# Performance work log

Hardware: AMD Instinct MI355X
Metric: run time of the kernel (lower is better)

Reference implementation:

```python
import jax, jax.numpy as jnp
import numpy as np

# Model dims: N = polynomial degree, RANK = CP rank, HxW image, S = flattened size
N, RANK, H, W = 4, 128, 256, 256
S = H * W
B = 32
EPS = 1e-5  # torch BatchNorm2d default eps


def setup_inputs() -> dict:
    key = jax.random.key(0)
    ks = jax.random.split(key, 4)
    x = jax.random.normal(ks[0], (B, 1, H, W), dtype=jnp.float32)
    # PolyLayer (PolyGAN CCP) parameters: per-degree factors U_n [S, RANK],
    # output projection C [S, RANK], output bias beta [S]
    U = jax.random.normal(ks[1], (N, S, RANK), dtype=jnp.float32) * 0.02
    C = jax.random.normal(ks[2], (S, RANK), dtype=jnp.float32) * 0.02
    beta = jax.random.normal(ks[3], (S,), dtype=jnp.float32) * 0.02
    # BatchNorm2d(1) affine params (torch default init: weight=1, bias=0)
    gamma = jnp.ones((1,), dtype=jnp.float32)
    bn_bias = jnp.zeros((1,), dtype=jnp.float32)
    return {"x": x, "U": U, "C": C, "beta": beta, "gamma": gamma, "bn_bias": bn_bias}


def reference(x, U, C, beta, gamma, bn_bias):
    b = x.shape[0]
    # BatchNorm2d(num_features=1), training mode: biased batch stats over (N,H,W)
    mean = jnp.mean(x, axis=(0, 2, 3), keepdims=True)
    var = jnp.var(x, axis=(0, 2, 3), keepdims=True)
    xn = (x - mean) * jax.lax.rsqrt(var + EPS)
    xn = xn * gamma.reshape(1, -1, 1, 1) + bn_bias.reshape(1, -1, 1, 1)
    # Flatten each sample: [B, S]. The torch Generator applies PolyLayer
    # per-sample across Python threads; here it is one batched call.
    z = xn.reshape(b, S)
    # CCP polynomial: t_n = U_n^T z for each degree -> [N, B, RANK]
    t = jnp.einsum('bs,nsr->nbr', z, U)
    h = t[0]
    for n in range(1, N):  # fixed small degree loop (structural, not data dim)
        h = t[n] * h + h   # h_n = (U_n^T z) * h_{n-1} + h_{n-1}
    out = h @ C.T + beta   # project back to image space: [B, S]
    return out.reshape(b, 1, H, W)
```

## Files before the change

### kernel.cpp

```cpp
#include <hip/hip_runtime.h>

#define SDIM 65536
#define BDIM 32
#define RDIM 128
#define NDEG 4
#define NCHUNK 256
#define CHUNK_S (SDIM / NCHUNK)
#define MTOT (BDIM * SDIM)
#define EPS_BN 1e-5f
#define NSTATB 512

__global__ void k_stats(const float* __restrict__ x, float* __restrict__ partial) {
    __shared__ float s_sum[256];
    __shared__ float s_sq[256];
    int tid = threadIdx.x;
    int gid = blockIdx.x * 256 + tid;
    int stride = gridDim.x * 256;
    float sum = 0.f, sq = 0.f;
    const float4* x4 = (const float4*)x;
    for (int i = gid; i < MTOT / 4; i += stride) {
        float4 v = x4[i];
        sum += (v.x + v.y) + (v.z + v.w);
        sq  += (v.x * v.x + v.y * v.y) + (v.z * v.z + v.w * v.w);
    }
    s_sum[tid] = sum; s_sq[tid] = sq;
    __syncthreads();
    for (int off = 128; off > 0; off >>= 1) {
        if (tid < off) { s_sum[tid] += s_sum[tid + off]; s_sq[tid] += s_sq[tid + off]; }
        __syncthreads();
    }
    if (tid == 0) { partial[blockIdx.x * 2] = s_sum[0]; partial[blockIdx.x * 2 + 1] = s_sq[0]; }
}

__global__ void k_stats_fin(const float* __restrict__ partial, float* __restrict__ stats) {
    __shared__ float s_sum[256];
    __shared__ float s_sq[256];
    int tid = threadIdx.x;
    float sum = partial[tid * 2] + partial[(tid + 256) * 2];
    float sq  = partial[tid * 2 + 1] + partial[(tid + 256) * 2 + 1];
    s_sum[tid] = sum; s_sq[tid] = sq;
    __syncthreads();
    for (int off = 128; off > 0; off >>= 1) {
        if (tid < off) { s_sum[tid] += s_sum[tid + off]; s_sq[tid] += s_sq[tid + off]; }
        __syncthreads();
    }
    if (tid == 0) { stats[0] = s_sum[0]; stats[1] = s_sq[0]; }
}

__global__ void __launch_bounds__(256) k_norm_t(const float* __restrict__ x,
                                                const float* __restrict__ gamma,
                                                const float* __restrict__ bnb,
                                                const float* __restrict__ stats,
                                                float* __restrict__ zT) {
    __shared__ float lds[64][33];
    int tid = threadIdx.x;
    int s0 = blockIdx.x * 64;
    float mean = stats[0] * (1.f / MTOT);
    float var  = stats[1] * (1.f / MTOT) - mean * mean;
    float istd = rsqrtf(var + EPS_BN);
    float a  = gamma[0] * istd;
    float c0 = bnb[0] - mean * a;

    int sl = tid & 63, bq = tid >> 6;
#pragma unroll
    for (int k = 0; k < 8; ++k) {
        int b = k * 4 + bq;
        lds[sl][b] = fmaf(a, x[(size_t)b * SDIM + s0 + sl], c0);
    }
    __syncthreads();
    int bl = tid & 31, sq = tid >> 5;
#pragma unroll
    for (int k = 0; k < 8; ++k) {
        int s = k * 8 + sq;
        zT[(size_t)(s0 + s) * BDIM + bl] = lds[s][bl];
    }
}

__global__ void __launch_bounds__(256) k_gemm_t(const float* __restrict__ zT,
                                                const float* __restrict__ U,
                                                float* __restrict__ t_part) {
    __shared__ float lds_z[CHUNK_S * BDIM];
    int tid  = threadIdx.x;
    int p    = tid & 63;
    int o    = __builtin_amdgcn_readfirstlane(tid >> 6);
    int chunk = blockIdx.x;
    int n     = blockIdx.y;
    int s0 = chunk * CHUNK_S;

    {
        const float4* src4 = (const float4*)(zT + (size_t)s0 * BDIM);
        float4* dst4 = (float4*)lds_z;
#pragma unroll
        for (int i = 0; i < (CHUNK_S * BDIM / 4) / 256; ++i)
            dst4[i * 256 + tid] = src4[i * 256 + tid];
    }
    __syncthreads();

    const float* Ub = U + (size_t)n * SDIM * RDIM + (size_t)s0 * RDIM;
    const float4* zq = (const float4*)lds_z;

    float acc[8][2];
#pragma unroll
    for (int j = 0; j < 8; ++j) { acc[j][0] = 0.f; acc[j][1] = 0.f; }

#pragma unroll 2
    for (int s = 0; s < CHUNK_S; ++s) {
        float4 z0 = zq[s * (BDIM / 4) + o * 2];
        float4 z1 = zq[s * (BDIM / 4) + o * 2 + 1];
        float2 u2 = *(const float2*)(Ub + (size_t)s * RDIM + 2 * p);
        acc[0][0] = fmaf(z0.x, u2.x, acc[0][0]); acc[0][1] = fmaf(z0.x, u2.y, acc[0][1]);
        acc[1][0] = fmaf(z0.y, u2.x, acc[1][0]); acc[1][1] = fmaf(z0.y, u2.y, acc[1][1]);
        acc[2][0] = fmaf(z0.z, u2.x, acc[2][0]); acc[2][1] = fmaf(z0.z, u2.y, acc[2][1]);
        acc[3][0] = fmaf(z0.w, u2.x, acc[3][0]); acc[3][1] = fmaf(z0.w, u2.y, acc[3][1]);
        acc[4][0] = fmaf(z1.x, u2.x, acc[4][0]); acc[4][1] = fmaf(z1.x, u2.y, acc[4][1]);
        acc[5][0] = fmaf(z1.y, u2.x, acc[5][0]); acc[5][1] = fmaf(z1.y, u2.y, acc[5][1]);
        acc[6][0] = fmaf(z1.z, u2.x, acc[6][0]); acc[6][1] = fmaf(z1.z, u2.y, acc[6][1]);
        acc[7][0] = fmaf(z1.w, u2.x, acc[7][0]); acc[7][1] = fmaf(z1.w, u2.y, acc[7][1]);
    }

    float* outp = t_part + ((size_t)n * NCHUNK + chunk) * (BDIM * RDIM);
#pragma unroll
    for (int j = 0; j < 8; ++j) {
        int b = o * 8 + j;
        *(float2*)(outp + b * RDIM + 2 * p) = make_float2(acc[j][0], acc[j][1]);
    }
}

__global__ void __launch_bounds__(256) k_reduce_h(const float* __restrict__ t_part,
                                                  float* __restrict__ h) {
    __shared__ float lds[NDEG][8][32];
    int tid = threadIdx.x;
    int il = tid & 31;
    int cg = tid >> 5;
    int i0 = blockIdx.x * 32;

#pragma unroll
    for (int n = 0; n < NDEG; ++n) {
        float s = 0.f;
#pragma unroll 4
        for (int k = 0; k < 32; ++k) {
            int c = cg * 32 + k;
            s += t_part[(size_t)(n * NCHUNK + c) * (BDIM * RDIM) + i0 + il];
        }
        lds[n][cg][il] = s;
    }
    __syncthreads();
    if (tid < 32) {
        float t[NDEG];
#pragma unroll
        for (int n = 0; n < NDEG; ++n) {
            float s = 0.f;
#pragma unroll
            for (int g = 0; g < 8; ++g) s += lds[n][g][il];
            t[n] = s;
        }
        float hh = t[0];
#pragma unroll
        for (int n = 1; n < NDEG; ++n) hh = fmaf(t[n], hh, hh);
        h[i0 + il] = hh;
    }
}

__global__ void __launch_bounds__(256) k_out(const float* __restrict__ h,
                                             const float* __restrict__ Cm,
                                             const float* __restrict__ beta,
                                             float* __restrict__ out) {
    int tid = threadIdx.x;
    int s   = (blockIdx.x >> 1) * 64 + (tid & 63);
    int bg  = __builtin_amdgcn_readfirstlane((blockIdx.x & 1) * 4 + (tid >> 6));
    int b0  = bg * 4;

    float acc[4] = {0.f, 0.f, 0.f, 0.f};
    const float4* Cr = (const float4*)(Cm + (size_t)s * RDIM);
    const float* hb = h + b0 * RDIM;

#pragma unroll 8
    for (int rc = 0; rc < RDIM / 4; ++rc) {
        float4 c = Cr[rc];
#pragma unroll
        for (int j = 0; j < 4; ++j) {
            const float* hr = hb + j * RDIM + rc * 4;
            float a = acc[j];
            a = fmaf(c.x, hr[0], a);
            a = fmaf(c.y, hr[1], a);
            a = fmaf(c.z, hr[2], a);
            a = fmaf(c.w, hr[3], a);
            acc[j] = a;
        }
    }
    float bt = beta[s];
#pragma unroll
    for (int j = 0; j < 4; ++j)
        out[(size_t)(b0 + j) * SDIM + s] = acc[j] + bt;
}

extern "C" void kernel_launch(void* const* d_in, const int* in_sizes, int n_in,
                              void* d_out, int out_size, void* d_ws, size_t ws_size,
                              hipStream_t stream) {
    const float* x     = (const float*)d_in[0];
    const float* U     = (const float*)d_in[1];
    const float* Cm    = (const float*)d_in[2];
    const float* beta  = (const float*)d_in[3];
    const float* gamma = (const float*)d_in[4];
    const float* bnb   = (const float*)d_in[5];
    float* out = (float*)d_out;

    char* ws = (char*)d_ws;
    size_t off = 0;
    float* stats   = (float*)(ws + off); off += 256;
    float* partial = (float*)(ws + off); off += NSTATB * 2 * 4;
    float* zT      = (float*)(ws + off); off += (size_t)BDIM * SDIM * 4;
    float* t_part  = (float*)(ws + off); off += (size_t)NDEG * NCHUNK * BDIM * RDIM * 4;
    float* h       = (float*)(ws + off); off += (size_t)BDIM * RDIM * 4;

    k_stats<<<NSTATB, 256, 0, stream>>>(x, partial);
    k_stats_fin<<<1, 256, 0, stream>>>(partial, stats);
    k_norm_t<<<SDIM / 64, 256, 0, stream>>>(x, gamma, bnb, stats, zT);
    dim3 g3(NCHUNK, NDEG);
    k_gemm_t<<<g3, 256, 0, stream>>>(zT, U, t_part);
    k_reduce_h<<<128, 256, 0, stream>>>(t_part, h);
    k_out<<<2048, 256, 0, stream>>>(h, Cm, beta, out);
}
```

Before: 111.7 us.

## Retile t-GEMM to 4x4 register blocks and double split-K chunk count

Changes the U^T z GEMM so each thread computes a 4-batch by 4-rank tile using float4 loads of U and z, batching four s-steps of loads ahead of the FMAs. This replaces the 8x2 per-thread tile, aiming for more arithmetic per load and wider memory accesses. NCHUNK goes from 256 to 512, which halves the work per block, doubles the number of blocks, and doubles the partial-sum buffer. The reduce kernel is updated to sum 64 chunks per group, so the t_part traffic written by the GEMM and read back by the reduction grows.

```diff
diff --git a/kernel.cpp b/kernel.cpp
--- a/kernel.cpp
+++ b/kernel.cpp
@@ -4,7 +4,7 @@
 #define BDIM 32
 #define RDIM 128
 #define NDEG 4
-#define NCHUNK 256
+#define NCHUNK 512
 #define CHUNK_S (SDIM / NCHUNK)
 #define MTOT (BDIM * SDIM)
 #define EPS_BN 1e-5f
@@ -81,8 +81,8 @@
                                                 float* __restrict__ t_part) {
     __shared__ float lds_z[CHUNK_S * BDIM];
     int tid  = threadIdx.x;
-    int p    = tid & 63;
-    int o    = __builtin_amdgcn_readfirstlane(tid >> 6);
+    int p    = tid & 31;
+    int o    = tid >> 5;
     int chunk = blockIdx.x;
     int n     = blockIdx.y;
     int s0 = chunk * CHUNK_S;
@@ -99,30 +99,46 @@
     const float* Ub = U + (size_t)n * SDIM * RDIM + (size_t)s0 * RDIM;
     const float4* zq = (const float4*)lds_z;
 
-    float acc[8][2];
-#pragma unroll
-    for (int j = 0; j < 8; ++j) { acc[j][0] = 0.f; acc[j][1] = 0.f; }
-
-#pragma unroll 2
-    for (int s = 0; s < CHUNK_S; ++s) {
-        float4 z0 = zq[s * (BDIM / 4) + o * 2];
-        float4 z1 = zq[s * (BDIM / 4) + o * 2 + 1];
-        float2 u2 = *(const float2*)(Ub + (size_t)s * RDIM + 2 * p);
-        acc[0][0] = fmaf(z0.x, u2.x, acc[0][0]); acc[0][1] = fmaf(z0.x, u2.y, acc[0][1]);
-        acc[1][0] = fmaf(z0.y, u2.x, acc[1][0]); acc[1][1] = fmaf(z0.y, u2.y, acc[1][1]);
-        acc[2][0] = fmaf(z0.z, u2.x, acc[2][0]); acc[2][1] = fmaf(z0.z, u2.y, acc[2][1]);
-        acc[3][0] = fmaf(z0.w, u2.x, acc[3][0]); acc[3][1] = fmaf(z0.w, u2.y, acc[3][1]);
-        acc[4][0] = fmaf(z1.x, u2.x, acc[4][0]); acc[4][1] = fmaf(z1.x, u2.y, acc[4][1]);
-        acc[5][0] = fmaf(z1.y, u2.x, acc[5][0]); acc[5][1] = fmaf(z1.y, u2.y, acc[5][1]);
-        acc[6][0] = fmaf(z1.z, u2.x, acc[6][0]); acc[6][1] = fmaf(z1.z, u2.y, acc[6][1]);
-        acc[7][0] = fmaf(z1.w, u2.x, acc[7][0]); acc[7][1] = fmaf(z1.w, u2.y, acc[7][1]);
+    float acc[4][4];
+#pragma unroll
+    for (int j = 0; j < 4; ++j)
+#pragma unroll
+        for (int k = 0; k < 4; ++k) acc[j][k] = 0.f;
+
+    for (int ss = 0; ss < CHUNK_S; ss += 4) {
+        float4 u[4], z[4];
+#pragma unroll
+        for (int k = 0; k < 4; ++k) {
+            u[k] = *(const float4*)(Ub + (size_t)(ss + k) * RDIM + 4 * p);
+            z[k] = zq[(ss + k) * (BDIM / 4) + o];
+        }
+#pragma unroll
+        for (int k = 0; k < 4; ++k) {
+            acc[0][0] = fmaf(z[k].x, u[k].x, acc[0][0]);
+            acc[0][1] = fmaf(z[k].x, u[k].y, acc[0][1]);
+            acc[0][2] = fmaf(z[k].x, u[k].z, acc[0][2]);
+            acc[0][3] = fmaf(z[k].x, u[k].w, acc[0][3]);
+            acc[1][0] = fmaf(z[k].y, u[k].x, acc[1][0]);
+            acc[1][1] = fmaf(z[k].y, u[k].y, acc[1][1]);
+            acc[1][2] = fmaf(z[k].y, u[k].z, acc[1][2]);
+            acc[1][3] = fmaf(z[k].y, u[k].w, acc[1][3]);
+            acc[2][0] = fmaf(z[k].z, u[k].x, acc[2][0]);
+            acc[2][1] = fmaf(z[k].z, u[k].y, acc[2][1]);
+            acc[2][2] = fmaf(z[k].z, u[k].z, acc[2][2]);
+            acc[2][3] = fmaf(z[k].z, u[k].w, acc[2][3]);
+            acc[3][0] = fmaf(z[k].w, u[k].x, acc[3][0]);
+            acc[3][1] = fmaf(z[k].w, u[k].y, acc[3][1]);
+            acc[3][2] = fmaf(z[k].w, u[k].z, acc[3][2]);
+            acc[3][3] = fmaf(z[k].w, u[k].w, acc[3][3]);
+        }
     }
 
     float* outp = t_part + ((size_t)n * NCHUNK + chunk) * (BDIM * RDIM);
 #pragma unroll
-    for (int j = 0; j < 8; ++j) {
-        int b = o * 8 + j;
-        *(float2*)(outp + b * RDIM + 2 * p) = make_float2(acc[j][0], acc[j][1]);
+    for (int j = 0; j < 4; ++j) {
+        int b = o * 4 + j;
+        *(float4*)(outp + b * RDIM + 4 * p) =
+            make_float4(acc[j][0], acc[j][1], acc[j][2], acc[j][3]);
     }
 }
 
@@ -137,9 +153,9 @@
 #pragma unroll
     for (int n = 0; n < NDEG; ++n) {
         float s = 0.f;
-#pragma unroll 4
-        for (int k = 0; k < 32; ++k) {
-            int c = cg * 32 + k;
+#pragma unroll 8
+        for (int k = 0; k < 64; ++k) {
+            int c = cg * 64 + k;
             s += t_part[(size_t)(n * NCHUNK + c) * (BDIM * RDIM) + i0 + il];
         }
         lds[n][cg][il] = s;
```

Result: no change. 111.9 us (+0.1%).
